# Kernel tuning notes

Measured on AMD Instinct MI355X. Metric: run time of the kernel, lower is better.

Reference implementation:

```python
import jax, jax.numpy as jnp
import numpy as np

B, U, D = 4096, 256, 128  # batch, units (classes), feature dim


def setup_inputs() -> dict:
    key = jax.random.key(0)
    kx, kw, kb = jax.random.split(key, 3)
    # Scale so points lie well inside the unit Poincare ball (c = 1).
    x = jax.random.normal(kx, (B, D), dtype=jnp.float32) * 0.05
    W = jax.random.normal(kw, (U, D), dtype=jnp.float32) * 0.05
    bias = (jax.random.uniform(kb, (U, D), dtype=jnp.float32) * 2.0 - 1.0) * 0.05
    return {"x": x, "W": W, "bias": bias}


def reference(x, W, bias):
    # c = 1 throughout (module hardcodes c = 1.0).
    def sqnorm(t):
        return jnp.sum(t * t, axis=-1, keepdims=True)

    nb2 = sqnorm(bias)                     # [U,1]  ||p_k||^2
    lam = 2.0 / (1.0 - nb2)                # [U,1]  lambda_{p_k}
    # parallel_transport: lambda_x(0)/lambda_x(bias) * W = (1 - ||bias||^2) * W
    a_k = (1.0 - nb2) * W                  # [U,D]
    a_norm = jnp.sqrt(sqnorm(a_k))         # [U,1]

    # mobius_add(-bias, x), broadcast instead of tiling x to [B,U,D]
    u = -bias[None, :, :]                  # [1,U,D]
    v = x[:, None, :]                      # [B,1,D]
    xy = jnp.sum(u * v, axis=-1, keepdims=True)   # [B,U,1]
    nu2 = nb2[None, :, :]                  # [1,U,1]
    nv2 = sqnorm(v)                        # [B,1,1]
    dd = 1.0 + 2.0 * xy + nu2 * nv2
    m = ((1.0 + 2.0 * xy + nv2) * u + (1.0 - nu2) * v) / dd   # [B,U,D]

    num = 2.0 * jnp.sum(m * a_k[None], axis=-1)               # [B,U]
    den = (1.0 - jnp.sum(m * m, axis=-1)) * a_norm[None, :, 0]  # [B,U]
    logits = (lam * a_norm)[None, :, 0] * jnp.arcsinh(num / den)  # [B,U]
    # exp(logits) / sum(exp(logits)) == softmax(logits) (stable form)
    return jax.nn.softmax(logits, axis=-1)
```

## Files before the change

kernel.cpp:

```cpp
#include <hip/hip_runtime.h>
#include <hip/hip_bf16.h>
#include <math.h>

#define BN 4096
#define UN 256
#define DN 128
#define MROW 16
#define BLOCK 256

typedef __attribute__((ext_vector_type(8))) short short8x;
typedef __attribute__((ext_vector_type(4))) float float4x;


__device__ inline ushort f2bf(float f) {
    __hip_bfloat16 h = __float2bfloat16(f);
    return *(ushort*)&h;
}
__device__ inline uint pack2bf(float a, float b) {
    return (uint)f2bf(a) | ((uint)f2bf(b) << 16);
}

__global__ __launch_bounds__(64) void prep_kernel(
    const float* __restrict__ W, const float* __restrict__ bias,
    ushort* __restrict__ Wb, ushort* __restrict__ Bb, float4* __restrict__ S)
{
    const int u = blockIdx.x;
    const int l = threadIdx.x;
    const float2 w2 = ((const float2*)(W    + (size_t)u * DN))[l];
    const float2 b2 = ((const float2*)(bias + (size_t)u * DN))[l];
    float nb2 = b2.x*b2.x + b2.y*b2.y;
    float bw  = b2.x*w2.x + b2.y*w2.y;
    float wn2 = w2.x*w2.x + w2.y*w2.y;
    #pragma unroll
    for (int off = 32; off; off >>= 1) {
        nb2 += __shfl_xor(nb2, off);
        bw  += __shfl_xor(bw , off);
        wn2 += __shfl_xor(wn2, off);
    }
    ((uint*)(Wb + (size_t)u * DN))[l] = pack2bf(w2.x, w2.y);
    ((uint*)(Bb + (size_t)u * DN))[l] = pack2bf(b2.x, b2.y);
    if (l == 0) S[u] = make_float4(nb2, bw, wn2, 0.f);
}

__global__ __launch_bounds__(BLOCK) void main_kernel(
    const float* __restrict__ x,
    const ushort* __restrict__ Wb, const ushort* __restrict__ Bb,
    const float4* __restrict__ S, float* __restrict__ out)
{
    __shared__ __align__(16) ushort xa[MROW][DN + 8];
    __shared__ float4 s_lds[UN];
    __shared__ float  nv2_lds[MROW];
    __shared__ float  logits[MROW][UN];

    const int t    = threadIdx.x;
    const int lane = t & 63;
    const int wave = t >> 6;
    const int b0   = blockIdx.x * MROW;

    s_lds[t] = S[t];

    {
        const int r = t >> 4, c = (t & 15) * 8;
        const float4* xp = (const float4*)(x + (size_t)(b0 + r) * DN + c);
        const float4 a = xp[0], b = xp[1];
        float sq = a.x*a.x + a.y*a.y + a.z*a.z + a.w*a.w
                 + b.x*b.x + b.y*b.y + b.z*b.z + b.w*b.w;
        uint4 p;
        p.x = pack2bf(a.x, a.y);  p.y = pack2bf(a.z, a.w);
        p.z = pack2bf(b.x, b.y);  p.w = pack2bf(b.z, b.w);
        *(uint4*)&xa[r][c] = p;
        #pragma unroll
        for (int off = 1; off < 16; off <<= 1) sq += __shfl_xor(sq, off);
        if ((t & 15) == 0) nv2_lds[r] = sq;
    }
    __syncthreads();

    const int m16 = lane & 15;
    const int q   = lane >> 4;
    float4x accW[4], accB[4];
    #pragma unroll
    for (int i = 0; i < 4; ++i)
        #pragma unroll
        for (int j = 0; j < 4; ++j) { accW[i][j] = 0.f; accB[i][j] = 0.f; }

    const ushort* xrow = &xa[m16][q * 8];
    #pragma unroll
    for (int ks = 0; ks < 4; ++ks) {
        const short8x afrag = *(const short8x*)(xrow + ks * 32);
        #pragma unroll
        for (int i = 0; i < 4; ++i) {
            const int u   = (wave * 4 + i) * 16 + m16;
            const int off = u * DN + ks * 32 + q * 8;
            const short8x wfrag = *(const short8x*)(Wb + off);
            const short8x bfrag = *(const short8x*)(Bb + off);
            accW[i] = __builtin_amdgcn_mfma_f32_16x16x32_bf16(afrag, wfrag, accW[i], 0, 0, 0);
            accB[i] = __builtin_amdgcn_mfma_f32_16x16x32_bf16(afrag, bfrag, accB[i], 0, 0, 0);
        }
    }

    #pragma unroll
    for (int i = 0; i < 4; ++i) {
        const int u = (wave * 4 + i) * 16 + m16;
        const float4 sc = s_lds[u];
        const float nb2 = sc.x, bw = sc.y, wn2 = sc.z;
        const float one_m  = 1.0f - nb2;
        const float a_norm = fabsf(one_m) * sqrtf(wn2);
        const float scale  = (2.0f / one_m) * a_norm;
        #pragma unroll
        for (int rg = 0; rg < 4; ++rg) {
            const int   mr   = q * 4 + rg;
            const float nv2  = nv2_lds[mr];
            const float dot1 = accW[i][rg];
            const float xy   = -accB[i][rg];
            const float dd   = 1.0f + 2.0f * xy + nb2 * nv2;
            const float inv_dd = __builtin_amdgcn_rcpf(dd);
            const float alpha  = (1.0f + 2.0f * xy + nv2) * inv_dd;
            const float beta   = one_m * inv_dd;
            const float num = 2.0f * one_m * (beta * dot1 - alpha * bw);
            const float mm  = alpha * alpha * nb2 + 2.0f * alpha * beta * xy
                            + beta * beta * nv2;
            const float den = (1.0f - mm) * a_norm;
            const float z   = num * __builtin_amdgcn_rcpf(den);
            const float s   = sqrtf(fmaf(z, z, 1.0f));
            logits[mr][u] = scale * copysignf(__logf(fabsf(z) + s), z);
        }
    }
    __syncthreads();

    for (int r = wave; r < MROW; r += 4) {
        float v0 = logits[r][lane];
        float v1 = logits[r][lane + 64];
        float v2 = logits[r][lane + 128];
        float v3 = logits[r][lane + 192];
        float mx = fmaxf(fmaxf(v0, v1), fmaxf(v2, v3));
        #pragma unroll
        for (int off = 32; off; off >>= 1) mx = fmaxf(mx, __shfl_xor(mx, off));
        float e0 = __expf(v0 - mx), e1 = __expf(v1 - mx);
        float e2 = __expf(v2 - mx), e3 = __expf(v3 - mx);
        float s = e0 + e1 + e2 + e3;
        #pragma unroll
        for (int off = 32; off; off >>= 1) s += __shfl_xor(s, off);
        const float inv = __builtin_amdgcn_rcpf(s);
        float* o = out + (size_t)(b0 + r) * UN;
        o[lane]       = e0 * inv;
        o[lane + 64]  = e1 * inv;
        o[lane + 128] = e2 * inv;
        o[lane + 192] = e3 * inv;
    }
}

extern "C" void kernel_launch(void* const* d_in, const int* in_sizes, int n_in,
                              void* d_out, int out_size, void* d_ws, size_t ws_size,
                              hipStream_t stream) {
    const float* x    = (const float*)d_in[0];
    const float* W    = (const float*)d_in[1];
    const float* bias = (const float*)d_in[2];
    float* out = (float*)d_out;

    ushort* Wb = (ushort*)d_ws;
    ushort* Bb = Wb + (size_t)UN * DN;
    float4* S  = (float4*)((char*)d_ws + 2 * (size_t)UN * DN * sizeof(ushort));

    hipLaunchKernelGGL(prep_kernel, dim3(UN), dim3(64), 0, stream, W, bias, Wb, Bb, S);
    hipLaunchKernelGGL(main_kernel, dim3(BN / MROW), dim3(BLOCK), 0, stream,
                       x, Wb, Bb, S, out);
}
```

Baseline: 68.76 us.

## Fuse prep into main kernel with 1024-thread blocks, one unit tile per wave

Removes the separate prep kernel and its workspace round-trip. Each block now runs 16 waves, each owning 16 units, and reads fp32 W and bias directly, converting them to bf16 and computing the per-unit norms in registers. x fragments are loaded straight from global into registers, and row norms are shared via shuffles instead of LDS. The softmax uses padded LDS rows and float4 stores. This saves one launch and the intermediate buffers, but every block re-reads and re-converts all of W and bias (256 blocks × 256 KB of fp32), which adds redundant global traffic and ALU work.

```diff
diff --git a/kernel.cpp b/kernel.cpp
--- a/kernel.cpp
+++ b/kernel.cpp
@@ -6,146 +6,131 @@
 #define UN 256
 #define DN 128
 #define MROW 16
-#define BLOCK 256
+#define BLOCK 1024
+#define LSTRIDE 260
 
 typedef __attribute__((ext_vector_type(8))) short short8x;
 typedef __attribute__((ext_vector_type(4))) float float4x;
 
-
-__device__ inline ushort f2bf(float f) {
-    __hip_bfloat16 h = __float2bfloat16(f);
-    return *(ushort*)&h;
-}
 __device__ inline uint pack2bf(float a, float b) {
-    return (uint)f2bf(a) | ((uint)f2bf(b) << 16);
+    __hip_bfloat16 ha = __float2bfloat16(a);
+    __hip_bfloat16 hb = __float2bfloat16(b);
+    return (uint)(*(ushort*)&ha) | ((uint)(*(ushort*)&hb) << 16);
 }
 
-__global__ __launch_bounds__(64) void prep_kernel(
-    const float* __restrict__ W, const float* __restrict__ bias,
-    ushort* __restrict__ Wb, ushort* __restrict__ Bb, float4* __restrict__ S)
+__global__ __launch_bounds__(BLOCK, 4) void fused_kernel(
+    const float* __restrict__ x,
+    const float* __restrict__ W,
+    const float* __restrict__ bias,
+    float* __restrict__ out)
 {
-    const int u = blockIdx.x;
-    const int l = threadIdx.x;
-    const float2 w2 = ((const float2*)(W    + (size_t)u * DN))[l];
-    const float2 b2 = ((const float2*)(bias + (size_t)u * DN))[l];
-    float nb2 = b2.x*b2.x + b2.y*b2.y;
-    float bw  = b2.x*w2.x + b2.y*w2.y;
-    float wn2 = w2.x*w2.x + w2.y*w2.y;
-    #pragma unroll
-    for (int off = 32; off; off >>= 1) {
-        nb2 += __shfl_xor(nb2, off);
-        bw  += __shfl_xor(bw , off);
-        wn2 += __shfl_xor(wn2, off);
-    }
-    ((uint*)(Wb + (size_t)u * DN))[l] = pack2bf(w2.x, w2.y);
-    ((uint*)(Bb + (size_t)u * DN))[l] = pack2bf(b2.x, b2.y);
-    if (l == 0) S[u] = make_float4(nb2, bw, wn2, 0.f);
-}
-
-__global__ __launch_bounds__(BLOCK) void main_kernel(
-    const float* __restrict__ x,
-    const ushort* __restrict__ Wb, const ushort* __restrict__ Bb,
-    const float4* __restrict__ S, float* __restrict__ out)
-{
-    __shared__ __align__(16) ushort xa[MROW][DN + 8];
-    __shared__ float4 s_lds[UN];
-    __shared__ float  nv2_lds[MROW];
-    __shared__ float  logits[MROW][UN];
+    __shared__ __align__(16) float logits[MROW][LSTRIDE];
 
     const int t    = threadIdx.x;
     const int lane = t & 63;
     const int wave = t >> 6;
+    const int m16  = lane & 15;
+    const int q    = lane >> 4;
     const int b0   = blockIdx.x * MROW;
+    const int u    = wave * 16 + m16;
 
-    s_lds[t] = S[t];
+    short8x afrag[4];
+    float sq = 0.f;
+    {
+        const float* xr = x + (size_t)(b0 + m16) * DN + q * 8;
+        #pragma unroll
+        for (int ks = 0; ks < 4; ++ks) {
+            const float4 a = *(const float4*)(xr + ks * 32);
+            const float4 b = *(const float4*)(xr + ks * 32 + 4);
+            sq = fmaf(a.x, a.x, sq); sq = fmaf(a.y, a.y, sq);
+            sq = fmaf(a.z, a.z, sq); sq = fmaf(a.w, a.w, sq);
+            sq = fmaf(b.x, b.x, sq); sq = fmaf(b.y, b.y, sq);
+            sq = fmaf(b.z, b.z, sq); sq = fmaf(b.w, b.w, sq);
+            uint4 p;
+            p.x = pack2bf(a.x, a.y);  p.y = pack2bf(a.z, a.w);
+            p.z = pack2bf(b.x, b.y);  p.w = pack2bf(b.z, b.w);
+            afrag[ks] = *(short8x*)&p;
+        }
+    }
+    sq += __shfl_xor(sq, 16);
+    sq += __shfl_xor(sq, 32);
 
+    short8x wfrag[4], bfrag[4];
+    float nb2 = 0.f, bw = 0.f, wn2 = 0.f;
     {
-        const int r = t >> 4, c = (t & 15) * 8;
-        const float4* xp = (const float4*)(x + (size_t)(b0 + r) * DN + c);
-        const float4 a = xp[0], b = xp[1];
-        float sq = a.x*a.x + a.y*a.y + a.z*a.z + a.w*a.w
-                 + b.x*b.x + b.y*b.y + b.z*b.z + b.w*b.w;
-        uint4 p;
-        p.x = pack2bf(a.x, a.y);  p.y = pack2bf(a.z, a.w);
-        p.z = pack2bf(b.x, b.y);  p.w = pack2bf(b.z, b.w);
-        *(uint4*)&xa[r][c] = p;
+        const float* wr = W    + (size_t)u * DN + q * 8;
+        const float* br = bias + (size_t)u * DN + q * 8;
         #pragma unroll
-        for (int off = 1; off < 16; off <<= 1) sq += __shfl_xor(sq, off);
-        if ((t & 15) == 0) nv2_lds[r] = sq;
+        for (int ks = 0; ks < 4; ++ks) {
+            const float4 w0 = *(const float4*)(wr + ks * 32);
+            const float4 w1 = *(const float4*)(wr + ks * 32 + 4);
+            const float4 c0 = *(const float4*)(br + ks * 32);
+            const float4 c1 = *(const float4*)(br + ks * 32 + 4);
+            nb2 = fmaf(c0.x,c0.x, fmaf(c0.y,c0.y, fmaf(c0.z,c0.z, fmaf(c0.w,c0.w,
+                  fmaf(c1.x,c1.x, fmaf(c1.y,c1.y, fmaf(c1.z,c1.z, fmaf(c1.w,c1.w, nb2))))))));
+            bw  = fmaf(c0.x,w0.x, fmaf(c0.y,w0.y, fmaf(c0.z,w0.z, fmaf(c0.w,w0.w,
+                  fmaf(c1.x,w1.x, fmaf(c1.y,w1.y, fmaf(c1.z,w1.z, fmaf(c1.w,w1.w, bw))))))));
+            wn2 = fmaf(w0.x,w0.x, fmaf(w0.y,w0.y, fmaf(w0.z,w0.z, fmaf(w0.w,w0.w,
+                  fmaf(w1.x,w1.x, fmaf(w1.y,w1.y, fmaf(w1.z,w1.z, fmaf(w1.w,w1.w, wn2))))))));
+            uint4 pw, pb;
+            pw.x = pack2bf(w0.x, w0.y);  pw.y = pack2bf(w0.z, w0.w);
+            pw.z = pack2bf(w1.x, w1.y);  pw.w = pack2bf(w1.z, w1.w);
+            pb.x = pack2bf(c0.x, c0.y);  pb.y = pack2bf(c0.z, c0.w);
+            pb.z = pack2bf(c1.x, c1.y);  pb.w = pack2bf(c1.z, c1.w);
+            wfrag[ks] = *(short8x*)&pw;
+            bfrag[ks] = *(short8x*)&pb;
+        }
+    }
+    nb2 += __shfl_xor(nb2, 16);  nb2 += __shfl_xor(nb2, 32);
+    bw  += __shfl_xor(bw , 16);  bw  += __shfl_xor(bw , 32);
+    wn2 += __shfl_xor(wn2, 16);  wn2 += __shfl_xor(wn2, 32);
+
+    float4x accW = {0.f, 0.f, 0.f, 0.f};
+    float4x accB = {0.f, 0.f, 0.f, 0.f};
+    #pragma unroll
+    for (int ks = 0; ks < 4; ++ks) {
+        accW = __builtin_amdgcn_mfma_f32_16x16x32_bf16(afrag[ks], wfrag[ks], accW, 0, 0, 0);
+        accB = __builtin_amdgcn_mfma_f32_16x16x32_bf16(afrag[ks], bfrag[ks], accB, 0, 0, 0);
+    }
+
+    const float one_m  = 1.0f - nb2;
+    const float a_norm = fabsf(one_m) * sqrtf(wn2);
+    const float scale  = (2.0f / one_m) * a_norm;
+    #pragma unroll
+    for (int rg = 0; rg < 4; ++rg) {
+        const int   mr   = q * 4 + rg;
+        const float nv2  = __shfl(sq, mr);
+        const float dot1 = accW[rg];
+        const float xy   = -accB[rg];
+        const float dd   = 1.0f + 2.0f * xy + nb2 * nv2;
+        const float inv_dd = __builtin_amdgcn_rcpf(dd);
+        const float alpha  = (1.0f + 2.0f * xy + nv2) * inv_dd;
+        const float beta   = one_m * inv_dd;
+        const float num = 2.0f * one_m * (beta * dot1 - alpha * bw);
+        const float mm  = alpha * alpha * nb2 + 2.0f * alpha * beta * xy
+                        + beta * beta * nv2;
+        const float den = (1.0f - mm) * a_norm;
+        const float z   = num * __builtin_amdgcn_rcpf(den);
+        const float s   = sqrtf(fmaf(z, z, 1.0f));
+        logits[mr][u] = scale * copysignf(__logf(fabsf(z) + s), z);
     }
     __syncthreads();
 
-    const int m16 = lane & 15;
-    const int q   = lane >> 4;
-    float4x accW[4], accB[4];
-    #pragma unroll
-    for (int i = 0; i < 4; ++i)
-        #pragma unroll
-        for (int j = 0; j < 4; ++j) { accW[i][j] = 0.f; accB[i][j] = 0.f; }
-
-    const ushort* xrow = &xa[m16][q * 8];
-    #pragma unroll
-    for (int ks = 0; ks < 4; ++ks) {
-        const short8x afrag = *(const short8x*)(xrow + ks * 32);
-        #pragma unroll
-        for (int i = 0; i < 4; ++i) {
-            const int u   = (wave * 4 + i) * 16 + m16;
-            const int off = u * DN + ks * 32 + q * 8;
-            const short8x wfrag = *(const short8x*)(Wb + off);
-            const short8x bfrag = *(const short8x*)(Bb + off);
-            accW[i] = __builtin_amdgcn_mfma_f32_16x16x32_bf16(afrag, wfrag, accW[i], 0, 0, 0);
-            accB[i] = __builtin_amdgcn_mfma_f32_16x16x32_bf16(afrag, bfrag, accB[i], 0, 0, 0);
-        }
-    }
-
-    #pragma unroll
-    for (int i = 0; i < 4; ++i) {
-        const int u = (wave * 4 + i) * 16 + m16;
-        const float4 sc = s_lds[u];
-        const float nb2 = sc.x, bw = sc.y, wn2 = sc.z;
-        const float one_m  = 1.0f - nb2;
-        const float a_norm = fabsf(one_m) * sqrtf(wn2);
-        const float scale  = (2.0f / one_m) * a_norm;
-        #pragma unroll
-        for (int rg = 0; rg < 4; ++rg) {
-            const int   mr   = q * 4 + rg;
-            const float nv2  = nv2_lds[mr];
-            const float dot1 = accW[i][rg];
-            const float xy   = -accB[i][rg];
-            const float dd   = 1.0f + 2.0f * xy + nb2 * nv2;
-            const float inv_dd = __builtin_amdgcn_rcpf(dd);
-            const float alpha  = (1.0f + 2.0f * xy + nv2) * inv_dd;
-            const float beta   = one_m * inv_dd;
-            const float num = 2.0f * one_m * (beta * dot1 - alpha * bw);
-            const float mm  = alpha * alpha * nb2 + 2.0f * alpha * beta * xy
-                            + beta * beta * nv2;
-            const float den = (1.0f - mm) * a_norm;
-            const float z   = num * __builtin_amdgcn_rcpf(den);
-            const float s   = sqrtf(fmaf(z, z, 1.0f));
-            logits[mr][u] = scale * copysignf(__logf(fabsf(z) + s), z);
-        }
-    }
-    __syncthreads();
-
-    for (int r = wave; r < MROW; r += 4) {
-        float v0 = logits[r][lane];
-        float v1 = logits[r][lane + 64];
-        float v2 = logits[r][lane + 128];
-        float v3 = logits[r][lane + 192];
-        float mx = fmaxf(fmaxf(v0, v1), fmaxf(v2, v3));
+    {
+        const int r = wave;
+        const float4 v = *(const float4*)&logits[r][lane * 4];
+        float mx = fmaxf(fmaxf(v.x, v.y), fmaxf(v.z, v.w));
         #pragma unroll
         for (int off = 32; off; off >>= 1) mx = fmaxf(mx, __shfl_xor(mx, off));
-        float e0 = __expf(v0 - mx), e1 = __expf(v1 - mx);
-        float e2 = __expf(v2 - mx), e3 = __expf(v3 - mx);
-        float s = e0 + e1 + e2 + e3;
+        float4 e;
+        e.x = __expf(v.x - mx);  e.y = __expf(v.y - mx);
+        e.z = __expf(v.z - mx);  e.w = __expf(v.w - mx);
+        float s = e.x + e.y + e.z + e.w;
         #pragma unroll
         for (int off = 32; off; off >>= 1) s += __shfl_xor(s, off);
         const float inv = __builtin_amdgcn_rcpf(s);
-        float* o = out + (size_t)(b0 + r) * UN;
-        o[lane]       = e0 * inv;
-        o[lane + 64]  = e1 * inv;
-        o[lane + 128] = e2 * inv;
-        o[lane + 192] = e3 * inv;
+        e.x *= inv;  e.y *= inv;  e.z *= inv;  e.w *= inv;
+        ((float4*)(out + (size_t)(b0 + r) * UN))[lane] = e;
     }
 }
 
@@ -156,12 +141,6 @@
     const float* W    = (const float*)d_in[1];
     const float* bias = (const float*)d_in[2];
     float* out = (float*)d_out;
-
-    ushort* Wb = (ushort*)d_ws;
-    ushort* Bb = Wb + (size_t)UN * DN;
-    float4* S  = (float4*)((char*)d_ws + 2 * (size_t)UN * DN * sizeof(ushort));
-
-    hipLaunchKernelGGL(prep_kernel, dim3(UN), dim3(64), 0, stream, W, bias, Wb, Bb, S);
-    hipLaunchKernelGGL(main_kernel, dim3(BN / MROW), dim3(BLOCK), 0, stream,
-                       x, Wb, Bb, S, out);
+    hipLaunchKernelGGL(fused_kernel, dim3(BN / MROW), dim3(BLOCK), 0, stream,
+                       x, W, bias, out);
 }
```

Measured after the change: 70.49 us. 2.5% more time.
